# Kernel tuning notes

Measured on AMD Instinct MI355X. Metric: run time of the kernel, lower is better.

Reference implementation:

```python
import jax, jax.numpy as jnp
import numpy as np

S, B, DIN, DBERT, H, L = 128, 32, 256, 768, 512, 2
NT_POS, NT_MORPH = 32, 64


def setup_inputs() -> dict:
    key = jax.random.key(0)
    ks = iter(jax.random.split(key, 32))
    def rn(shape, s=0.1):
        return jax.random.normal(next(ks), shape, dtype=jnp.float32) * s
    D0 = DIN + DBERT  # 1024 == 2*H, so per-layer LSTM weights stack cleanly
    return {
        "src_segments": rn((S, B, DIN), 1.0),
        "bert_encodings": rn((B, DBERT), 1.0),
        "labels_pos": jax.random.randint(next(ks), (S, B), 0, NT_POS, dtype=jnp.int32),
        "labels_morph": jax.random.randint(next(ks), (S, B), 0, NT_MORPH, dtype=jnp.int32),
        # stacked LSTM params: [layer, direction, ...], PyTorch gate order i,f,g,o
        "w_ih": rn((L, 2, 4 * H, D0)),
        "w_hh": rn((L, 2, 4 * H, H)),
        "b_ih": rn((L, 2, 4 * H)),
        "b_hh": rn((L, 2, 4 * H)),
        "head_w_pos": rn((NT_POS, 2 * H)),
        "head_b_pos": rn((NT_POS,)),
        "head_w_morph": rn((NT_MORPH, 2 * H)),
        "head_b_morph": rn((NT_MORPH,)),
        "start_pos": rn((NT_POS,)), "end_pos": rn((NT_POS,)), "trans_pos": rn((NT_POS, NT_POS)),
        "start_morph": rn((NT_MORPH,)), "end_morph": rn((NT_MORPH,)), "trans_morph": rn((NT_MORPH, NT_MORPH)),
    }


def _run_dir(x, w_ih, w_hh, b):
    # x: [S, B, D]; one LSTM direction via scan over time
    bsz, hd = x.shape[1], w_hh.shape[1]
    def step(carry, xt):
        h, c = carry
        g = xt @ w_ih.T + h @ w_hh.T + b  # [B, 4H]
        i, f, gg, o = jnp.split(g, 4, axis=-1)
        c = jax.nn.sigmoid(f) * c + jax.nn.sigmoid(i) * jnp.tanh(gg)
        h = jax.nn.sigmoid(o) * jnp.tanh(c)
        return (h, c), h
    init = (jnp.zeros((bsz, hd), x.dtype), jnp.zeros((bsz, hd), x.dtype))
    _, hs = jax.lax.scan(step, init, x)
    return hs


def _bilstm(x, w_ih, w_hh, b_ih, b_hh):
    out = x
    for l in range(w_ih.shape[0]):
        b = b_ih[l] + b_hh[l]
        fwd = _run_dir(out, w_ih[l, 0], w_hh[l, 0], b[0])
        bwd = _run_dir(out[::-1], w_ih[l, 1], w_hh[l, 1], b[1])[::-1]
        out = jnp.concatenate([fwd, bwd], axis=-1)  # [S, B, 2H]
    return out


def _crf_ll(em, tags, start, trans, end):
    # torchcrf log-likelihood, mask=None, reduction='sum'. em: [S,B,K], tags: [S,B]
    bsz = em.shape[1]
    first = start[tags[0]] + em[0, jnp.arange(bsz), tags[0]]
    em_sc = jnp.take_along_axis(em, tags[..., None], axis=2)[..., 0]  # [S,B]
    num = first + trans[tags[:-1], tags[1:]].sum(0) + em_sc[1:].sum(0) + end[tags[-1]]
    def step(alpha, et):  # alpha: [B,K]
        return jax.nn.logsumexp(alpha[:, :, None] + trans[None], axis=1) + et, None
    alpha, _ = jax.lax.scan(step, start[None, :] + em[0], em[1:])
    den = jax.nn.logsumexp(alpha + end[None, :], axis=1)
    return jnp.sum(num - den)


def reference(src_segments, bert_encodings, labels_pos, labels_morph,
              w_ih, w_hh, b_ih, b_hh,
              head_w_pos, head_b_pos, head_w_morph, head_b_morph,
              start_pos, end_pos, trans_pos, start_morph, end_morph, trans_morph):
    # bert encodings are repeated over seq and concatenated on features
    bert = jnp.broadcast_to(bert_encodings[None], (src_segments.shape[0],) + bert_encodings.shape)
    emb = jnp.concatenate([src_segments, bert], axis=-1)  # dropout p=0 -> identity
    out = _bilstm(emb, w_ih, w_hh, b_ih, b_hh)            # [S,B,2H]
    feat_pos = out @ head_w_pos.T + head_b_pos            # [S,B,32]
    feat_morph = out @ head_w_morph.T + head_b_morph      # [S,B,64]
    ll = (_crf_ll(feat_pos, labels_pos, start_pos, trans_pos, end_pos)
          + _crf_ll(feat_morph, labels_morph, start_morph, trans_morph, end_morph))
    return -ll  # loss = -sum_f crf_f(emissions_f, labels_f)
```

## Files before the change

kernel.cpp:

```cpp
#include <hip/hip_runtime.h>


typedef unsigned short u16;
typedef unsigned long long u64;
typedef __attribute__((ext_vector_type(8))) __bf16 bf16x8;
typedef __attribute__((ext_vector_type(4))) float floatx4;

static __device__ __forceinline__ u16 f2bf(float f) {
  unsigned int u = __float_as_uint(f);
  u += 0x7fffu + ((u >> 16) & 1u);
  return (u16)(u >> 16);
}
static __device__ __forceinline__ float sigf(float x) {
  return 1.0f / (1.0f + __expf(-x));
}
static __device__ __forceinline__ float tanh_(float x) {
  return 1.0f - 2.0f / (1.0f + __expf(2.0f * x));
}
static __device__ __forceinline__ floatx4 mfma16(bf16x8 a, bf16x8 b, floatx4 c) {
  return __builtin_amdgcn_mfma_f32_16x16x32_bf16(a, b, c, 0, 0, 0);
}

__global__ __launch_bounds__(256) void prep_kernel(
    const float* __restrict__ w_ih, const float* __restrict__ w_hh,
    const float* __restrict__ b_ih, const float* __restrict__ b_hh,
    const float* __restrict__ src,  const float* __restrict__ bert,
    const float* __restrict__ hwp,  const float* __restrict__ hbp,
    const float* __restrict__ hwm,  const float* __restrict__ hbm,
    u16* __restrict__ Wsrc, u16* __restrict__ Wbert, u16* __restrict__ Wih1,
    u16* __restrict__ Whh,  u16* __restrict__ SrcBf, u16* __restrict__ BertBf,
    u16* __restrict__ Wheads, float* __restrict__ b0sum, float* __restrict__ b1sum,
    float* __restrict__ hb, float* __restrict__ dout, int* __restrict__ bar)
{
  const int NA = 4194304;
  const int NB = 4194304;
  const int NC = 4194304;
  const int ND = 1048576;
  const int NE = 24576;
  const int NF = 98304;
  const int NG = 8192;
  const int NH = 96;
  const int TOTAL = NA + NB + NC + ND + NE + NF + NG + NH + 1 + 64;
  for (int i = blockIdx.x * 256 + threadIdx.x; i < TOTAL; i += gridDim.x * 256) {
    int x = i;
    if (x < NA) {
      int c = x & 1023, r = x >> 10;
      float v = w_ih[x];
      if (c < 256) Wsrc[r * 256 + c] = f2bf(v);
      else         Wbert[r * 768 + (c - 256)] = f2bf(v);
      continue;
    }
    x -= NA;
    if (x < NB) { Wih1[x] = f2bf(w_ih[NA + x]); continue; }
    x -= NB;
    if (x < NC) { Whh[x] = f2bf(w_hh[x]); continue; }
    x -= NC;
    if (x < ND) { SrcBf[x] = f2bf(src[x]); continue; }
    x -= ND;
    if (x < NE) { BertBf[x] = f2bf(bert[x]); continue; }
    x -= NE;
    if (x < NF) {
      Wheads[x] = f2bf(x < 32768 ? hwp[x] : hwm[x - 32768]);
      continue;
    }
    x -= NF;
    if (x < NG) {
      float v = b_ih[x] + b_hh[x];
      if (x < 4096) b0sum[x] = v; else b1sum[x - 4096] = v;
      continue;
    }
    x -= NG;
    if (x < NH) { hb[x] = (x < 32) ? hbp[x] : hbm[x - 32]; continue; }
    x -= NH;
    if (x == 0) { dout[0] = 0.f; continue; }
    x -= 1;
    bar[x] = 0;
  }
}

__global__ __launch_bounds__(256) void gemm_nt(
    const u16* __restrict__ A, int lda,
    const u16* __restrict__ B, int ldb,
    float* __restrict__ C, int ldc,
    int M, int N, int K,
    const float* __restrict__ bias_n,
    const float* __restrict__ auxBN, int auxld,
    int n_split, long dir_stride)
{
  __shared__ __align__(16) u16 As[128 * 64];
  __shared__ __align__(16) u16 Bs[128 * 64];
  const int m0 = blockIdx.y * 128, n0 = blockIdx.x * 128;
  const int tid = threadIdx.x;
  const int wv = tid >> 6, ln = tid & 63;
  const int wm = wv & 1, wn = wv >> 1;
  const int q = ln >> 4, l15 = ln & 15;
  floatx4 acc[4][4];
#pragma unroll
  for (int a = 0; a < 4; ++a)
#pragma unroll
    for (int b2 = 0; b2 < 4; ++b2) acc[a][b2] = (floatx4){0.f, 0.f, 0.f, 0.f};

  for (int kk = 0; kk < K; kk += 64) {
    __syncthreads();
#pragma unroll
    for (int j = 0; j < 4; ++j) {
      const int idx = j * 256 + tid;
      const int r = idx >> 3, cc = idx & 7;
      const int slot = cc ^ (r & 7);
      const int ra = min(m0 + r, M - 1);
      *(int4*)&As[r * 64 + slot * 8] = *(const int4*)&A[(long)ra * lda + kk + cc * 8];
      const int rb = min(n0 + r, N - 1);
      *(int4*)&Bs[r * 64 + slot * 8] = *(const int4*)&B[(long)rb * ldb + kk + cc * 8];
    }
    __syncthreads();
#pragma unroll
    for (int ks = 0; ks < 2; ++ks) {
      bf16x8 af[4], bf[4];
#pragma unroll
      for (int im = 0; im < 4; ++im) {
        const int r = wm * 64 + im * 16 + l15;
        const int slot = (ks * 4 + q) ^ (r & 7);
        af[im] = *(const bf16x8*)&As[r * 64 + slot * 8];
      }
#pragma unroll
      for (int jn = 0; jn < 4; ++jn) {
        const int r = wn * 64 + jn * 16 + l15;
        const int slot = (ks * 4 + q) ^ (r & 7);
        bf[jn] = *(const bf16x8*)&Bs[r * 64 + slot * 8];
      }
#pragma unroll
      for (int im = 0; im < 4; ++im)
#pragma unroll
        for (int jn = 0; jn < 4; ++jn)
          acc[im][jn] = mfma16(af[im], bf[jn], acc[im][jn]);
    }
  }
#pragma unroll
  for (int im = 0; im < 4; ++im)
#pragma unroll
    for (int jn = 0; jn < 4; ++jn) {
      const int n = n0 + wn * 64 + jn * 16 + l15;
      if (n < N) {
        const int dirsel = (n >= n_split) ? 1 : 0;
        const long cb = (long)dirsel * dir_stride - (long)dirsel * n_split + n;
        const float badd = bias_n ? bias_n[n] : 0.f;
#pragma unroll
        for (int rg = 0; rg < 4; ++rg) {
          const int m = m0 + wm * 64 + im * 16 + q * 4 + rg;
          if (m < M) {
            float v = acc[im][jn][rg] + badd;
            if (auxBN) v += auxBN[(long)(m & 31) * auxld + n];
            C[cb + (long)m * ldc] = v;
          }
        }
      }
    }
}

__global__ __launch_bounds__(256) void lstm_rec(
    const float* __restrict__ gates,
    u16* __restrict__ out,
    const u16* __restrict__ whh,
    int* __restrict__ bar,
    int tbase)
{
  __shared__ __align__(16) u16 h_lds[16 * 512];
  __shared__ float gsc[4][16][17];
  const int bid = blockIdx.x;
  const int dir = bid >> 6;
  const int mh = (bid >> 5) & 1;
  const int grp = bid >> 5;
  int* cnt = bar + grp * 16;
  const int u0 = (bid & 31) * 16;
  const int tid = threadIdx.x;
  const int wv = tid >> 6;
  const int ln = tid & 63;
  const int q = ln >> 4, l15 = ln & 15;

  const int gate_r = (l15 >> 2) * 512 + u0 + wv * 4 + (l15 & 3);

  bf16x8 bfrag[16];
  {
    const u16* wp = whh + ((long)dir * 2048 + gate_r) * 512 + q * 8;
#pragma unroll
    for (int ks = 0; ks < 16; ++ks)
      bfrag[ks] = *(const bf16x8*)(wp + ks * 32);
  }

  float c = 0.f;
  const int j_lane = u0 + wv * 4 + q;
  const int b_glob = mh * 16 + l15;

  const float* gbase = gates + (((long)dir * 128) * 32 + mh * 16) * 2048 + gate_r;

  float g4[4];
  {
    const float* gp = gbase + (long)(dir ? 127 : 0) * 65536;
#pragma unroll
    for (int rg = 0; rg < 4; ++rg) g4[rg] = gp[(q * 4 + rg) * 2048];
  }

  for (int t = 0; t < 128; ++t) {
    const int s = dir ? (127 - t) : t;
    float g4n[4];
    if (t < 127) {
      const int sn = dir ? (126 - t) : (t + 1);
      const float* gp = gbase + (long)sn * 65536;
#pragma unroll
      for (int rg = 0; rg < 4; ++rg) g4n[rg] = gp[(q * 4 + rg) * 2048];
    }
    if (t > 0) {
      if (tid == 0) {
        const int target = tbase + 32 * t;
        while (__hip_atomic_load(cnt, __ATOMIC_RELAXED, __HIP_MEMORY_SCOPE_AGENT) < target)
          __builtin_amdgcn_s_sleep(1);
      }
      __syncthreads();
      const int sp = dir ? (s + 1) : (s - 1);
      const u64* ub = (const u64*)(out + (((long)sp * 32 + mh * 16) * 1024 + (long)dir * 512));
      u64 v8[8];
#pragma unroll
      for (int j = 0; j < 8; ++j) {
        const int idx = j * 256 + tid;
        const int r = idx >> 7, c4 = idx & 127;
        v8[j] = __hip_atomic_load((u64*)(ub + (long)r * 256 + c4),
                                  __ATOMIC_RELAXED, __HIP_MEMORY_SCOPE_AGENT);
      }
#pragma unroll
      for (int j = 0; j < 8; ++j) {
        const int idx = j * 256 + tid;
        const int r = idx >> 7, c4 = idx & 127;
        const int cc8 = c4 >> 1, hf = c4 & 1;
        *(u64*)&h_lds[r * 512 + ((cc8 ^ (r & 7)) << 3) + (hf << 2)] = v8[j];
      }
      __syncthreads();
    }
    floatx4 acc = (floatx4){0.f, 0.f, 0.f, 0.f};
    if (t > 0) {
      floatx4 acc1 = (floatx4){0.f, 0.f, 0.f, 0.f};
#pragma unroll
      for (int ks = 0; ks < 16; ks += 2) {
        const int slot0 = (ks * 4 + q) ^ (l15 & 7);
        bf16x8 a0 = *(const bf16x8*)&h_lds[l15 * 512 + slot0 * 8];
        acc = mfma16(a0, bfrag[ks], acc);
        const int slot1 = ((ks + 1) * 4 + q) ^ (l15 & 7);
        bf16x8 a1 = *(const bf16x8*)&h_lds[l15 * 512 + slot1 * 8];
        acc1 = mfma16(a1, bfrag[ks + 1], acc1);
      }
      acc += acc1;
    }
#pragma unroll
    for (int rg = 0; rg < 4; ++rg)
      gsc[wv][q * 4 + rg][l15] = acc[rg] + g4[rg];
    __syncthreads();
    const float gi = gsc[wv][l15][q];
    const float gf = gsc[wv][l15][4 + q];
    const float gg = gsc[wv][l15][8 + q];
    const float go = gsc[wv][l15][12 + q];
    const float iv = sigf(gi), fv = sigf(gf), gv = tanh_(gg), ov = sigf(go);
    c = fv * c + iv * gv;
    const float h = ov * tanh_(c);
    const u16 hv = f2bf(h);
    const unsigned int up = (unsigned int)__shfl_xor((int)(unsigned int)hv, 16);
    if ((q & 1) == 0) {
      const unsigned int pk = (unsigned int)hv | (up << 16);
      __hip_atomic_store(
          (unsigned int*)&out[((long)s * 32 + b_glob) * 1024 + dir * 512 + j_lane],
          pk, __ATOMIC_RELAXED, __HIP_MEMORY_SCOPE_AGENT);
    }
#pragma unroll
    for (int rg = 0; rg < 4; ++rg) g4[rg] = g4n[rg];
    if (t < 127) {
      __syncthreads();
      if (tid == 0)
        __hip_atomic_fetch_add(cnt, 1, __ATOMIC_RELAXED, __HIP_MEMORY_SCOPE_AGENT);
    }
  }
}

template <int K>
static __device__ void crf_body(const float* __restrict__ feat, int off,
                                const int* __restrict__ labels, int b,
                                const float* __restrict__ start,
                                const float* __restrict__ end_,
                                const float* __restrict__ trans,
                                float* __restrict__ outp,
                                float* transT, float* alpha, float* red)
{
  const int tid = threadIdx.x;
  for (int i = tid; i < K * K; i += 256) {
    int kk = i / K, kp2 = i % K;
    transT[kp2 * 65 + kk] = trans[i];
  }
  if (tid < K) alpha[tid] = start[tid] + feat[b * 96 + off + tid];
  __syncthreads();
  constexpr int Kq = K / 4;
  const int kp = tid >> 2, k4 = tid & 3;
  const bool act = kp < K;
  for (int s = 1; s < 128; ++s) {
    float x[Kq];
    float mx = -3e38f;
    if (act) {
      const float* tr = &transT[kp * 65 + k4 * Kq];
      const float* al = &alpha[k4 * Kq];
#pragma unroll
      for (int i2 = 0; i2 < Kq; ++i2) { x[i2] = al[i2] + tr[i2]; mx = fmaxf(mx, x[i2]); }
    }
    mx = fmaxf(mx, __shfl_xor(mx, 1));
    mx = fmaxf(mx, __shfl_xor(mx, 2));
    float ss = 0.f;
    if (act) {
#pragma unroll
      for (int i2 = 0; i2 < Kq; ++i2) ss += __expf(x[i2] - mx);
    }
    ss += __shfl_xor(ss, 1);
    ss += __shfl_xor(ss, 2);
    const float nv = mx + __logf(ss) + feat[(s * 32 + b) * 96 + off + kp];
    __syncthreads();
    if (act && k4 == 0) alpha[kp] = nv;
    __syncthreads();
  }
  float term = 0.f;
  if (tid < 128) {
    const int tg = labels[tid * 32 + b];
    term = feat[(tid * 32 + b) * 96 + off + tg];
    if (tid == 0) term += start[tg];
    else          term += trans[labels[(tid - 1) * 32 + b] * K + tg];
    if (tid == 127) term += end_[tg];
    red[tid] = term;
  }
  __syncthreads();
  if (tid == 0) {
    float num = 0.f;
    for (int i = 0; i < 128; ++i) num += red[i];
    float mx = -3e38f;
    for (int k = 0; k < K; ++k) mx = fmaxf(mx, alpha[k] + end_[k]);
    float ss = 0.f;
    for (int k = 0; k < K; ++k) ss += __expf(alpha[k] + end_[k] - mx);
    const float den = mx + __logf(ss);
    atomicAdd(outp, den - num);
  }
}

__global__ __launch_bounds__(256) void crf_kernel(
    const float* __restrict__ feat,
    const int* __restrict__ labp, const int* __restrict__ labm,
    const float* __restrict__ stp, const float* __restrict__ enp, const float* __restrict__ trp,
    const float* __restrict__ stm, const float* __restrict__ enm, const float* __restrict__ trm,
    float* __restrict__ outp)
{
  __shared__ float transT[64 * 65];
  __shared__ float alpha[64];
  __shared__ float red[128];
  const int task = blockIdx.x >> 5, b = blockIdx.x & 31;
  if (task == 0) crf_body<32>(feat, 0,  labp, b, stp, enp, trp, outp, transT, alpha, red);
  else           crf_body<64>(feat, 32, labm, b, stm, enm, trm, outp, transT, alpha, red);
}

extern "C" void kernel_launch(void* const* d_in, const int* in_sizes, int n_in,
                              void* d_out, int out_size, void* d_ws, size_t ws_size,
                              hipStream_t stream) {
  const float* src  = (const float*)d_in[0];
  const float* bert = (const float*)d_in[1];
  const int*   labp = (const int*)d_in[2];
  const int*   labm = (const int*)d_in[3];
  const float* w_ih = (const float*)d_in[4];
  const float* w_hh = (const float*)d_in[5];
  const float* b_ih = (const float*)d_in[6];
  const float* b_hh = (const float*)d_in[7];
  const float* hwp  = (const float*)d_in[8];
  const float* hbp  = (const float*)d_in[9];
  const float* hwm  = (const float*)d_in[10];
  const float* hbm  = (const float*)d_in[11];
  const float* stp  = (const float*)d_in[12];
  const float* enp  = (const float*)d_in[13];
  const float* trp  = (const float*)d_in[14];
  const float* stm  = (const float*)d_in[15];
  const float* enm  = (const float*)d_in[16];
  const float* trm  = (const float*)d_in[17];

  char* ws = (char*)d_ws;
  u16*   Wsrc     = (u16*)(ws + 0);
  u16*   Wbert    = (u16*)(ws + 2097152);
  u16*   Wih1     = (u16*)(ws + 8388608);
  u16*   Whh      = (u16*)(ws + 16777216);
  u16*   SrcBf    = (u16*)(ws + 25165824);
  u16*   BertBf   = (u16*)(ws + 27262976);
  u16*   Wheads   = (u16*)(ws + 27312128);
  float* b0sum    = (float*)(ws + 27508736);
  float* b1sum    = (float*)(ws + 27525120);
  float* hb       = (float*)(ws + 27541504);
  int*   bar      = (int*)(ws + 27542016);
  float* bertpart = (float*)(ws + 27542272);
  float* feat     = (float*)(ws + 28066560);
  u16*   out0     = (u16*)(ws + 29639424);
  u16*   out1     = (u16*)(ws + 38028032);
  float* gates    = (float*)(ws + 46416640);
  float* dout     = (float*)d_out;

  hipLaunchKernelGGL(prep_kernel, dim3(2048), dim3(256), 0, stream,
      w_ih, w_hh, b_ih, b_hh, src, bert, hwp, hbp, hwm, hbm,
      Wsrc, Wbert, Wih1, Whh, SrcBf, BertBf, Wheads, b0sum, b1sum, hb, dout, bar);

  hipLaunchKernelGGL(gemm_nt, dim3(32, 1), dim3(256), 0, stream,
      BertBf, 768, Wbert, 768, bertpart, 4096, 32, 4096, 768,
      b0sum, (const float*)nullptr, 0, 1 << 30, 0L);

  hipLaunchKernelGGL(gemm_nt, dim3(32, 32), dim3(256), 0, stream,
      SrcBf, 256, Wsrc, 256, gates, 2048, 4096, 4096, 256,
      (const float*)nullptr, bertpart, 4096, 2048, (long)(4096L * 2048L));

  {
    const float* g = gates; u16* o = out0; const u16* wh = Whh; int* bp = bar; int tb = 0;
    void* args[] = {&g, &o, &wh, &bp, &tb};
    hipLaunchCooperativeKernel(reinterpret_cast<void*>(&lstm_rec),
                               dim3(128), dim3(256), args, 0, stream);
  }

  hipLaunchKernelGGL(gemm_nt, dim3(32, 32), dim3(256), 0, stream,
      out0, 1024, Wih1, 1024, gates, 2048, 4096, 4096, 1024,
      b1sum, (const float*)nullptr, 0, 2048, (long)(4096L * 2048L));

  {
    const float* g = gates; u16* o = out1; const u16* wh = Whh + 2L * 2048 * 512;
    int* bp = bar; int tb = 4064;
    void* args[] = {&g, &o, &wh, &bp, &tb};
    hipLaunchCooperativeKernel(reinterpret_cast<void*>(&lstm_rec),
                               dim3(128), dim3(256), args, 0, stream);
  }

  hipLaunchKernelGGL(gemm_nt, dim3(1, 32), dim3(256), 0, stream,
      out1, 1024, Wheads, 1024, feat, 96, 4096, 96, 1024,
      hb, (const float*)nullptr, 0, 1 << 30, 0L);

  hipLaunchKernelGGL(crf_kernel, dim3(64), dim3(256), 0, stream,
      feat, labp, labm, stp, enp, trp, stm, enm, trm, dout);
}
```

Before: 1.025 ms.

## Replace block counter barrier with per-wave flags and direct global h loads

The recurrent LSTM kernel drops the per-group atomic counter and the LDS staging of the previous hidden state. Each wave now publishes its own step flag after its h store drains. Consumer waves spin on all 128 flags of their group with vectorised loads and then read their MFMA A-fragments straight from global memory. Several __syncthreads are removed, including the one between the gsc scratch write and read, which is now only valid within a wave. This trims barrier and LDS latency on the serial critical path, at the cost of more polling traffic and redundant global reads per wave.

```diff
diff --git a/kernel.cpp b/kernel.cpp
--- a/kernel.cpp
+++ b/kernel.cpp
@@ -40,7 +40,7 @@
   const int NF = 98304;
   const int NG = 8192;
   const int NH = 96;
-  const int TOTAL = NA + NB + NC + ND + NE + NF + NG + NH + 1 + 64;
+  const int TOTAL = NA + NB + NC + ND + NE + NF + NG + NH + 1 + 512;
   for (int i = blockIdx.x * 256 + threadIdx.x; i < TOTAL; i += gridDim.x * 256) {
     int x = i;
     if (x < NA) {
@@ -157,20 +157,18 @@
     }
 }
 
-__global__ __launch_bounds__(256) void lstm_rec(
+__global__ __launch_bounds__(256, 1) void lstm_rec(
     const float* __restrict__ gates,
     u16* __restrict__ out,
     const u16* __restrict__ whh,
-    int* __restrict__ bar,
+    int* __restrict__ flags,
     int tbase)
 {
-  __shared__ __align__(16) u16 h_lds[16 * 512];
   __shared__ float gsc[4][16][17];
   const int bid = blockIdx.x;
   const int dir = bid >> 6;
   const int mh = (bid >> 5) & 1;
   const int grp = bid >> 5;
-  int* cnt = bar + grp * 16;
   const int u0 = (bid & 31) * 16;
   const int tid = threadIdx.x;
   const int wv = tid >> 6;
@@ -188,10 +186,13 @@
   }
 
   float c = 0.f;
-  const int j_lane = u0 + wv * 4 + q;
   const int b_glob = mh * 16 + l15;
 
   const float* gbase = gates + (((long)dir * 128) * 32 + mh * 16) * 2048 + gate_r;
+
+  int* myflag = flags + (grp * 32 + (bid & 31)) * 4 + wv;
+  const u64* fl = (const u64*)(flags + grp * 128);
+  const int li = ln & 31;
 
   float g4[4];
   {
@@ -209,50 +210,40 @@
 #pragma unroll
       for (int rg = 0; rg < 4; ++rg) g4n[rg] = gp[(q * 4 + rg) * 2048];
     }
-    if (t > 0) {
-      if (tid == 0) {
-        const int target = tbase + 32 * t;
-        while (__hip_atomic_load(cnt, __ATOMIC_RELAXED, __HIP_MEMORY_SCOPE_AGENT) < target)
-          __builtin_amdgcn_s_sleep(1);
-      }
-      __syncthreads();
-      const int sp = dir ? (s + 1) : (s - 1);
-      const u64* ub = (const u64*)(out + (((long)sp * 32 + mh * 16) * 1024 + (long)dir * 512));
-      u64 v8[8];
-#pragma unroll
-      for (int j = 0; j < 8; ++j) {
-        const int idx = j * 256 + tid;
-        const int r = idx >> 7, c4 = idx & 127;
-        v8[j] = __hip_atomic_load((u64*)(ub + (long)r * 256 + c4),
-                                  __ATOMIC_RELAXED, __HIP_MEMORY_SCOPE_AGENT);
-      }
-#pragma unroll
-      for (int j = 0; j < 8; ++j) {
-        const int idx = j * 256 + tid;
-        const int r = idx >> 7, c4 = idx & 127;
-        const int cc8 = c4 >> 1, hf = c4 & 1;
-        *(u64*)&h_lds[r * 512 + ((cc8 ^ (r & 7)) << 3) + (hf << 2)] = v8[j];
-      }
-      __syncthreads();
-    }
     floatx4 acc = (floatx4){0.f, 0.f, 0.f, 0.f};
     if (t > 0) {
+      const int target = tbase + t;
+      while (true) {
+        u64 a = __hip_atomic_load(fl + li * 2,     __ATOMIC_RELAXED, __HIP_MEMORY_SCOPE_AGENT);
+        u64 b = __hip_atomic_load(fl + li * 2 + 1, __ATOMIC_RELAXED, __HIP_MEMORY_SCOPE_AGENT);
+        int m0 = min((int)(unsigned int)(a & 0xffffffffu), (int)(unsigned int)(a >> 32));
+        int m1 = min((int)(unsigned int)(b & 0xffffffffu), (int)(unsigned int)(b >> 32));
+        if (__all(min(m0, m1) >= target)) break;
+      }
+      const int sp = dir ? (s + 1) : (s - 1);
+      const u64* ap = (const u64*)(out + ((long)(sp * 32 + mh * 16 + l15) * 1024 + dir * 512));
+      u64 va[32];
+#pragma unroll
+      for (int ks = 0; ks < 16; ++ks) {
+        va[2 * ks]     = __hip_atomic_load(ap + ks * 8 + q * 2,
+                                           __ATOMIC_RELAXED, __HIP_MEMORY_SCOPE_AGENT);
+        va[2 * ks + 1] = __hip_atomic_load(ap + ks * 8 + q * 2 + 1,
+                                           __ATOMIC_RELAXED, __HIP_MEMORY_SCOPE_AGENT);
+      }
       floatx4 acc1 = (floatx4){0.f, 0.f, 0.f, 0.f};
 #pragma unroll
       for (int ks = 0; ks < 16; ks += 2) {
-        const int slot0 = (ks * 4 + q) ^ (l15 & 7);
-        bf16x8 a0 = *(const bf16x8*)&h_lds[l15 * 512 + slot0 * 8];
-        acc = mfma16(a0, bfrag[ks], acc);
-        const int slot1 = ((ks + 1) * 4 + q) ^ (l15 & 7);
-        bf16x8 a1 = *(const bf16x8*)&h_lds[l15 * 512 + slot1 * 8];
-        acc1 = mfma16(a1, bfrag[ks + 1], acc1);
+        union { u64 u[2]; bf16x8 v; } c0, c1;
+        c0.u[0] = va[2 * ks];     c0.u[1] = va[2 * ks + 1];
+        acc = mfma16(c0.v, bfrag[ks], acc);
+        c1.u[0] = va[2 * ks + 2]; c1.u[1] = va[2 * ks + 3];
+        acc1 = mfma16(c1.v, bfrag[ks + 1], acc1);
       }
       acc += acc1;
     }
 #pragma unroll
     for (int rg = 0; rg < 4; ++rg)
       gsc[wv][q * 4 + rg][l15] = acc[rg] + g4[rg];
-    __syncthreads();
     const float gi = gsc[wv][l15][q];
     const float gf = gsc[wv][l15][4 + q];
     const float gg = gsc[wv][l15][8 + q];
@@ -260,20 +251,22 @@
     const float iv = sigf(gi), fv = sigf(gf), gv = tanh_(gg), ov = sigf(go);
     c = fv * c + iv * gv;
     const float h = ov * tanh_(c);
-    const u16 hv = f2bf(h);
-    const unsigned int up = (unsigned int)__shfl_xor((int)(unsigned int)hv, 16);
-    if ((q & 1) == 0) {
-      const unsigned int pk = (unsigned int)hv | (up << 16);
+    const unsigned int hv = (unsigned int)f2bf(h);
+    const unsigned int p1 = (unsigned int)__shfl_xor((int)hv, 16);
+    const unsigned int lo32 = hv | (p1 << 16);
+    const u64 w64 = (u64)lo32 |
+                    ((u64)(unsigned int)__shfl_xor((int)lo32, 32) << 32);
+    if (q == 0)
       __hip_atomic_store(
-          (unsigned int*)&out[((long)s * 32 + b_glob) * 1024 + dir * 512 + j_lane],
-          pk, __ATOMIC_RELAXED, __HIP_MEMORY_SCOPE_AGENT);
-    }
+          (u64*)&out[((long)s * 32 + b_glob) * 1024 + dir * 512 + u0 + wv * 4],
+          w64, __ATOMIC_RELAXED, __HIP_MEMORY_SCOPE_AGENT);
 #pragma unroll
     for (int rg = 0; rg < 4; ++rg) g4[rg] = g4n[rg];
     if (t < 127) {
-      __syncthreads();
-      if (tid == 0)
-        __hip_atomic_fetch_add(cnt, 1, __ATOMIC_RELAXED, __HIP_MEMORY_SCOPE_AGENT);
+      asm volatile("s_waitcnt vmcnt(0)" ::: "memory");
+      if (ln == 0)
+        __hip_atomic_store(myflag, tbase + t + 1,
+                           __ATOMIC_RELAXED, __HIP_MEMORY_SCOPE_AGENT);
     }
   }
 }
@@ -390,17 +383,17 @@
   float* b0sum    = (float*)(ws + 27508736);
   float* b1sum    = (float*)(ws + 27525120);
   float* hb       = (float*)(ws + 27541504);
-  int*   bar      = (int*)(ws + 27542016);
   float* bertpart = (float*)(ws + 27542272);
   float* feat     = (float*)(ws + 28066560);
   u16*   out0     = (u16*)(ws + 29639424);
   u16*   out1     = (u16*)(ws + 38028032);
   float* gates    = (float*)(ws + 46416640);
+  int*   flags    = (int*)(ws + 113525504);
   float* dout     = (float*)d_out;
 
   hipLaunchKernelGGL(prep_kernel, dim3(2048), dim3(256), 0, stream,
       w_ih, w_hh, b_ih, b_hh, src, bert, hwp, hbp, hwm, hbm,
-      Wsrc, Wbert, Wih1, Whh, SrcBf, BertBf, Wheads, b0sum, b1sum, hb, dout, bar);
+      Wsrc, Wbert, Wih1, Whh, SrcBf, BertBf, Wheads, b0sum, b1sum, hb, dout, flags);
 
   hipLaunchKernelGGL(gemm_nt, dim3(32, 1), dim3(256), 0, stream,
       BertBf, 768, Wbert, 768, bertpart, 4096, 32, 4096, 768,
@@ -411,7 +404,7 @@
       (const float*)nullptr, bertpart, 4096, 2048, (long)(4096L * 2048L));
 
   {
-    const float* g = gates; u16* o = out0; const u16* wh = Whh; int* bp = bar; int tb = 0;
+    const float* g = gates; u16* o = out0; const u16* wh = Whh; int* bp = flags; int tb = 0;
     void* args[] = {&g, &o, &wh, &bp, &tb};
     hipLaunchCooperativeKernel(reinterpret_cast<void*>(&lstm_rec),
                                dim3(128), dim3(256), args, 0, stream);
@@ -423,7 +416,7 @@
 
   {
     const float* g = gates; u16* o = out1; const u16* wh = Whh + 2L * 2048 * 512;
-    int* bp = bar; int tb = 4064;
+    int* bp = flags; int tb = 127;
     void* args[] = {&g, &o, &wh, &bp, &tb};
     hipLaunchCooperativeKernel(reinterpret_cast<void*>(&lstm_rec),
                                dim3(128), dim3(256), args, 0, stream);
```

Result: slower. 2.301 ms (+124.4%).
